# Performance work log

Hardware: AMD Instinct MI355X
Metric: run time of the kernel (lower is better)

## Reference

```python
import jax, jax.numpy as jnp
import numpy as np
from jax import lax

ALPHA = 1.5
N_ITER = 50  # entmax bisect default
GAIN = 1.414


def _p(z):
    # gp_inv(clamp(z,0), alpha) = z_+^(1/(alpha-1)) = z_+^2 for alpha=1.5
    zc = jnp.clip(z, 0.0, None)
    return zc * zc


def entmax15(X):
    """alpha-entmax (alpha=1.5) along last dim via bisection (entmax lib algorithm)."""
    d = X.shape[-1]
    Xs = X * (ALPHA - 1.0)
    mx = jnp.max(Xs, axis=-1, keepdims=True)
    tau_lo = mx - 1.0                       # gp(1, alpha) = 1
    tau_hi = mx - (1.0 / d) ** (ALPHA - 1.0)  # gp(1/d, alpha)
    f_lo = jnp.sum(_p(Xs - tau_lo), axis=-1, keepdims=True) - 1.0

    def body(i, carry):
        tau_lo, dm = carry
        dm = dm * 0.5
        tau_m = tau_lo + dm
        f_m = jnp.sum(_p(Xs - tau_m), axis=-1, keepdims=True) - 1.0
        tau_lo = jnp.where(f_m * f_lo >= 0.0, tau_m, tau_lo)
        return (tau_lo, dm)

    tau_lo, _ = lax.fori_loop(0, N_ITER, body, (tau_lo, tau_hi - tau_lo))
    p = _p(Xs - tau_lo)
    return p / jnp.sum(p, axis=-1, keepdims=True)  # ensure_sum_one=True


def _xavier(key, shape):
    std = GAIN * (2.0 / (shape[0] + shape[1])) ** 0.5
    a = (3.0 ** 0.5) * std
    return jax.random.uniform(key, shape, minval=-a, maxval=a, dtype=jnp.float32)


def setup_inputs() -> dict:
    B, F, E, N = 2048, 64, 256, 64  # batch, nfield, nemb, ncross
    key = jax.random.key(0)
    k1, k2, k3, k4 = jax.random.split(key, 4)
    return {
        "x": jax.random.normal(k1, (B, F, E), dtype=jnp.float32),
        "bilinear_w": _xavier(k2, (E, E)),
        "query": _xavier(k3, (N, E)),
        "value": _xavier(k4, (N, F)),
    }


def reference(x, bilinear_w, query, value):
    # x: [B,F,E]; bilinear_w: [E,E]; query: [N,E]; value: [N,F]
    scale = x.shape[-1] ** -0.5
    k = jnp.einsum('bfe,de->bfd', x, bilinear_w)        # [B,F,E]
    att_gate = jnp.einsum('bfd,nd->bnf', k, query) * scale  # [B,N,F]
    sparse_gate = entmax15(att_gate)                     # entmax over F
    attn_weight = sparse_gate * value[None]              # [B,N,F]
    return jnp.exp(jnp.einsum('bfe,bnf->bne', x, attn_weight))  # [B,N,E]
```

## Files before the change

kernel.cpp:

```cpp
#include <hip/hip_runtime.h>
#include <hip/hip_bf16.h>

typedef __attribute__((ext_vector_type(8))) short bf16x8;
typedef __attribute__((ext_vector_type(4))) float f32x4;

__device__ __forceinline__ unsigned short f2bf(float f) {
  unsigned int u = __float_as_uint(f);
  u += 0x7FFFu + ((u >> 16) & 1u);
  return (unsigned short)(u >> 16);
}

__global__ void __launch_bounds__(256) qw_kernel(const float* __restrict__ q,
                                                 const float* __restrict__ W,
                                                 unsigned short* __restrict__ qw) {
  int n = blockIdx.x, e = threadIdx.x;
  float acc = 0.f;
  #pragma unroll 8
  for (int d = 0; d < 256; ++d) acc = fmaf(q[n * 256 + d], W[d * 256 + e], acc);
  qw[n * 256 + e] = f2bf(acc * 0.0625f);
}

__global__ void __launch_bounds__(512, 6) cross_main(
    const float* __restrict__ x, const float* __restrict__ value,
    const unsigned short* __restrict__ qw, float* __restrict__ out) {

  __shared__ __align__(16) unsigned short lds_x[64 * 264];
  __shared__ __align__(16) unsigned char  lds_pool[64 * 68 * 4];

  float* lds_att = (float*)lds_pool;
  unsigned short* lds_aw = (unsigned short*)lds_pool;

  const int t = threadIdx.x;
  const int b = blockIdx.x;
  const int l = t & 63;
  const int w = t >> 6;
  const int l15 = l & 15, l4 = l >> 4;

  {
    const float4* xg = (const float4*)(x + (size_t)b * 16384);
    #pragma unroll
    for (int it = 0; it < 8; ++it) {
      int i = it * 512 + t;
      float4 v = xg[i];
      int f = i >> 6, c = i & 63;
      unsigned int lo = (unsigned int)f2bf(v.x) | ((unsigned int)f2bf(v.y) << 16);
      unsigned int hi = (unsigned int)f2bf(v.z) | ((unsigned int)f2bf(v.w) << 16);
      *(uint2*)&lds_x[f * 264 + 4 * c] = make_uint2(lo, hi);
    }
  }
  __syncthreads();

  {
    int nt = w >> 1, ft0 = (w & 1) * 2;
    f32x4 acc0 = {0.f, 0.f, 0.f, 0.f}, acc1 = {0.f, 0.f, 0.f, 0.f};
    const unsigned short* qa = qw + (nt * 16 + l15) * 256 + l4 * 8;
    const unsigned short* xb0 = &lds_x[(ft0 * 16 + l15) * 264 + l4 * 8];
    const unsigned short* xb1 = xb0 + 16 * 264;
    #pragma unroll
    for (int kc = 0; kc < 8; ++kc) {
      bf16x8 a  = *(const bf16x8*)(qa + kc * 32);
      bf16x8 b0 = *(const bf16x8*)(xb0 + kc * 32);
      bf16x8 b1 = *(const bf16x8*)(xb1 + kc * 32);
      acc0 = __builtin_amdgcn_mfma_f32_16x16x32_bf16(a, b0, acc0, 0, 0, 0);
      acc1 = __builtin_amdgcn_mfma_f32_16x16x32_bf16(a, b1, acc1, 0, 0, 0);
    }
    int nrow = nt * 16 + 4 * l4;
    #pragma unroll
    for (int r = 0; r < 4; ++r) {
      lds_att[(nrow + r) * 68 + ft0 * 16 + l15]       = acc0[r];
      lds_att[(nrow + r) * 68 + (ft0 + 1) * 16 + l15] = acc1[r];
    }
  }
  __syncthreads();

  {
    int n = w * 8 + (l >> 3);
    int fb = (l & 7) * 8;
    f32x4 z0 = *(const f32x4*)&lds_att[n * 68 + fb];
    f32x4 z1 = *(const f32x4*)&lds_att[n * 68 + fb + 4];
    __syncthreads();
    float z[8];
    #pragma unroll
    for (int k = 0; k < 4; ++k) { z[k] = z0[k] * 0.5f; z[k + 4] = z1[k] * 0.5f; }
    float m = z[0];
    #pragma unroll
    for (int k = 1; k < 8; ++k) m = fmaxf(m, z[k]);
    m = fmaxf(m, __shfl_xor(m, 1));
    m = fmaxf(m, __shfl_xor(m, 2));
    m = fmaxf(m, __shfl_xor(m, 4));
    float tau = m - 1.0f;
    float dm = (m - 0.125f) - tau;
    float s = 0.f;
    #pragma unroll
    for (int k = 0; k < 8; ++k) { float d = fmaxf(z[k] - tau, 0.f); s = fmaf(d, d, s); }
    s += __shfl_xor(s, 1); s += __shfl_xor(s, 2); s += __shfl_xor(s, 4);
    const float f_lo = s - 1.0f;
    for (int it = 0; it < 28; ++it) {
      dm *= 0.5f;
      float tm = tau + dm;
      float s2 = 0.f;
      #pragma unroll
      for (int k = 0; k < 8; ++k) { float d = fmaxf(z[k] - tm, 0.f); s2 = fmaf(d, d, s2); }
      s2 += __shfl_xor(s2, 1); s2 += __shfl_xor(s2, 2); s2 += __shfl_xor(s2, 4);
      if ((s2 - 1.0f) * f_lo >= 0.f) tau = tm;
    }
    float p[8]; float S = 0.f;
    #pragma unroll
    for (int k = 0; k < 8; ++k) { float d = fmaxf(z[k] - tau, 0.f); p[k] = d * d; S += p[k]; }
    S += __shfl_xor(S, 1); S += __shfl_xor(S, 2); S += __shfl_xor(S, 4);
    float invS = 1.0f / S;
    const float4* vg = (const float4*)(value + n * 64 + fb);
    float4 va = vg[0], vb = vg[1];
    union { unsigned short u[8]; bf16x8 v; } pk;
    pk.u[0] = f2bf(p[0] * invS * va.x); pk.u[1] = f2bf(p[1] * invS * va.y);
    pk.u[2] = f2bf(p[2] * invS * va.z); pk.u[3] = f2bf(p[3] * invS * va.w);
    pk.u[4] = f2bf(p[4] * invS * vb.x); pk.u[5] = f2bf(p[5] * invS * vb.y);
    pk.u[6] = f2bf(p[6] * invS * vb.z); pk.u[7] = f2bf(p[7] * invS * vb.w);
    *(bf16x8*)&lds_aw[n * 72 + fb] = pk.v;
  }
  __syncthreads();

  {
    const int te0 = 2 * w;
    f32x4 acc[4][2];
    #pragma unroll
    for (int nt = 0; nt < 4; ++nt) {
      acc[nt][0] = (f32x4){0.f, 0.f, 0.f, 0.f};
      acc[nt][1] = (f32x4){0.f, 0.f, 0.f, 0.f};
    }
    #pragma unroll
    for (int kc = 0; kc < 2; ++kc) {
      bf16x8 a[4];
      #pragma unroll
      for (int nt = 0; nt < 4; ++nt)
        a[nt] = *(const bf16x8*)&lds_aw[(nt * 16 + l15) * 72 + kc * 32 + l4 * 8];
      int f0 = kc * 32 + l4 * 8;
      #pragma unroll
      for (int j = 0; j < 2; ++j) {
        int e = (te0 + j) * 16 + l15;
        union { unsigned short u[8]; bf16x8 v; } bb;
        #pragma unroll
        for (int i = 0; i < 8; ++i) bb.u[i] = lds_x[(f0 + i) * 264 + e];
        #pragma unroll
        for (int nt = 0; nt < 4; ++nt)
          acc[nt][j] = __builtin_amdgcn_mfma_f32_16x16x32_bf16(a[nt], bb.v, acc[nt][j], 0, 0, 0);
      }
    }
    float* ob = out + (size_t)b * 16384;
    #pragma unroll
    for (int nt = 0; nt < 4; ++nt) {
      #pragma unroll
      for (int j = 0; j < 2; ++j) {
        #pragma unroll
        for (int r = 0; r < 4; ++r) {
          ob[(nt * 16 + 4 * l4 + r) * 256 + (te0 + j) * 16 + l15] = __expf(acc[nt][j][r]);
        }
      }
    }
  }
}

extern "C" void kernel_launch(void* const* d_in, const int* in_sizes, int n_in,
                              void* d_out, int out_size, void* d_ws, size_t ws_size,
                              hipStream_t stream) {
  const float* x     = (const float*)d_in[0];
  const float* W     = (const float*)d_in[1];
  const float* q     = (const float*)d_in[2];
  const float* value = (const float*)d_in[3];
  float* out = (float*)d_out;
  unsigned short* qw = (unsigned short*)d_ws;

  qw_kernel<<<dim3(64), dim3(256), 0, stream>>>(q, W, qw);
  cross_main<<<dim3(2048), dim3(512), 0, stream>>>(x, value, qw, out);
}
```

Measured before the change: 76.92 us.

## Replace entmax bisection with Newton iterations and repad x LDS tile

The 28-step bisection for the entmax threshold becomes 12 Newton-style updates. Each update uses the sum of squares and the linear sum of the clipped differences, so there are fewer iterations and fewer shuffle reductions per row. The x tile in LDS gets a row stride of 268 instead of 264, with matching 8-byte loads and stores to change bank-conflict patterns. Float-to-bf16 conversion switches to the packed intrinsic. Newton convergence from the lower bound with only 12 steps may give a threshold that differs slightly from the bisection result.

```diff
diff --git a/kernel.cpp b/kernel.cpp
--- a/kernel.cpp
+++ b/kernel.cpp
@@ -4,6 +4,11 @@
 typedef __attribute__((ext_vector_type(8))) short bf16x8;
 typedef __attribute__((ext_vector_type(4))) float f32x4;
 
+__device__ __forceinline__ unsigned int pk2(float a, float b) {
+  union { __hip_bfloat162 h; unsigned int u; } cv;
+  cv.h = __float22bfloat162_rn(make_float2(a, b));
+  return cv.u;
+}
 __device__ __forceinline__ unsigned short f2bf(float f) {
   unsigned int u = __float_as_uint(f);
   u += 0x7FFFu + ((u >> 16) & 1u);
@@ -24,7 +29,7 @@
     const float* __restrict__ x, const float* __restrict__ value,
     const unsigned short* __restrict__ qw, float* __restrict__ out) {
 
-  __shared__ __align__(16) unsigned short lds_x[64 * 264];
+  __shared__ __align__(16) unsigned short lds_x[64 * 268];
   __shared__ __align__(16) unsigned char  lds_pool[64 * 68 * 4];
 
   float* lds_att = (float*)lds_pool;
@@ -39,13 +44,13 @@
   {
     const float4* xg = (const float4*)(x + (size_t)b * 16384);
     #pragma unroll
-    for (int it = 0; it < 8; ++it) {
-      int i = it * 512 + t;
-      float4 v = xg[i];
-      int f = i >> 6, c = i & 63;
-      unsigned int lo = (unsigned int)f2bf(v.x) | ((unsigned int)f2bf(v.y) << 16);
-      unsigned int hi = (unsigned int)f2bf(v.z) | ((unsigned int)f2bf(v.w) << 16);
-      *(uint2*)&lds_x[f * 264 + 4 * c] = make_uint2(lo, hi);
+    for (int it = 0; it < 4; ++it) {
+      int u = it * 512 + t;
+      float4 v0 = xg[2 * u], v1 = xg[2 * u + 1];
+      int f = u >> 5, c8 = u & 31;
+      char* dst = (char*)lds_x + f * 536 + c8 * 16;
+      *(uint2*)dst       = make_uint2(pk2(v0.x, v0.y), pk2(v0.z, v0.w));
+      *(uint2*)(dst + 8) = make_uint2(pk2(v1.x, v1.y), pk2(v1.z, v1.w));
     }
   }
   __syncthreads();
@@ -54,15 +59,19 @@
     int nt = w >> 1, ft0 = (w & 1) * 2;
     f32x4 acc0 = {0.f, 0.f, 0.f, 0.f}, acc1 = {0.f, 0.f, 0.f, 0.f};
     const unsigned short* qa = qw + (nt * 16 + l15) * 256 + l4 * 8;
-    const unsigned short* xb0 = &lds_x[(ft0 * 16 + l15) * 264 + l4 * 8];
-    const unsigned short* xb1 = xb0 + 16 * 264;
+    const char* rb0 = (const char*)lds_x + (ft0 * 16 + l15) * 536 + l4 * 16;
+    const char* rb1 = rb0 + 16 * 536;
     #pragma unroll
     for (int kc = 0; kc < 8; ++kc) {
-      bf16x8 a  = *(const bf16x8*)(qa + kc * 32);
-      bf16x8 b0 = *(const bf16x8*)(xb0 + kc * 32);
-      bf16x8 b1 = *(const bf16x8*)(xb1 + kc * 32);
-      acc0 = __builtin_amdgcn_mfma_f32_16x16x32_bf16(a, b0, acc0, 0, 0, 0);
-      acc1 = __builtin_amdgcn_mfma_f32_16x16x32_bf16(a, b1, acc1, 0, 0, 0);
+      union BF { uint2 d[2]; bf16x8 v; };
+      bf16x8 a = *(const bf16x8*)(qa + kc * 32);
+      BF b0, b1;
+      b0.d[0] = *(const uint2*)(rb0 + kc * 64);
+      b0.d[1] = *(const uint2*)(rb0 + kc * 64 + 8);
+      b1.d[0] = *(const uint2*)(rb1 + kc * 64);
+      b1.d[1] = *(const uint2*)(rb1 + kc * 64 + 8);
+      acc0 = __builtin_amdgcn_mfma_f32_16x16x32_bf16(a, b0.v, acc0, 0, 0, 0);
+      acc1 = __builtin_amdgcn_mfma_f32_16x16x32_bf16(a, b1.v, acc1, 0, 0, 0);
     }
     int nrow = nt * 16 + 4 * l4;
     #pragma unroll
@@ -82,27 +91,26 @@
     float z[8];
     #pragma unroll
     for (int k = 0; k < 4; ++k) { z[k] = z0[k] * 0.5f; z[k + 4] = z1[k] * 0.5f; }
-    float m = z[0];
-    #pragma unroll
-    for (int k = 1; k < 8; ++k) m = fmaxf(m, z[k]);
+    float m = fmaxf(fmaxf(fmaxf(z[0], z[1]), fmaxf(z[2], z[3])),
+                    fmaxf(fmaxf(z[4], z[5]), fmaxf(z[6], z[7])));
     m = fmaxf(m, __shfl_xor(m, 1));
     m = fmaxf(m, __shfl_xor(m, 2));
     m = fmaxf(m, __shfl_xor(m, 4));
     float tau = m - 1.0f;
-    float dm = (m - 0.125f) - tau;
-    float s = 0.f;
     #pragma unroll
-    for (int k = 0; k < 8; ++k) { float d = fmaxf(z[k] - tau, 0.f); s = fmaf(d, d, s); }
-    s += __shfl_xor(s, 1); s += __shfl_xor(s, 2); s += __shfl_xor(s, 4);
-    const float f_lo = s - 1.0f;
-    for (int it = 0; it < 28; ++it) {
-      dm *= 0.5f;
-      float tm = tau + dm;
-      float s2 = 0.f;
+    for (int it = 0; it < 12; ++it) {
+      float s0 = 0.f, s1 = 0.f, q0 = 0.f, q1 = 0.f;
       #pragma unroll
-      for (int k = 0; k < 8; ++k) { float d = fmaxf(z[k] - tm, 0.f); s2 = fmaf(d, d, s2); }
-      s2 += __shfl_xor(s2, 1); s2 += __shfl_xor(s2, 2); s2 += __shfl_xor(s2, 4);
-      if ((s2 - 1.0f) * f_lo >= 0.f) tau = tm;
+      for (int k = 0; k < 4; ++k) {
+        float d0 = fmaxf(z[k] - tau, 0.f);
+        float d1 = fmaxf(z[k + 4] - tau, 0.f);
+        s0 = fmaf(d0, d0, s0); q0 += d0;
+        s1 = fmaf(d1, d1, s1); q1 += d1;
+      }
+      float s = s0 + s1, q = q0 + q1;
+      s += __shfl_xor(s, 1); s += __shfl_xor(s, 2); s += __shfl_xor(s, 4);
+      q += __shfl_xor(q, 1); q += __shfl_xor(q, 2); q += __shfl_xor(q, 4);
+      tau += (s - 1.0f) * 0.5f * __builtin_amdgcn_rcpf(q);
     }
     float p[8]; float S = 0.f;
     #pragma unroll
@@ -111,12 +119,12 @@
     float invS = 1.0f / S;
     const float4* vg = (const float4*)(value + n * 64 + fb);
     float4 va = vg[0], vb = vg[1];
-    union { unsigned short u[8]; bf16x8 v; } pk;
-    pk.u[0] = f2bf(p[0] * invS * va.x); pk.u[1] = f2bf(p[1] * invS * va.y);
-    pk.u[2] = f2bf(p[2] * invS * va.z); pk.u[3] = f2bf(p[3] * invS * va.w);
-    pk.u[4] = f2bf(p[4] * invS * vb.x); pk.u[5] = f2bf(p[5] * invS * vb.y);
-    pk.u[6] = f2bf(p[6] * invS * vb.z); pk.u[7] = f2bf(p[7] * invS * vb.w);
-    *(bf16x8*)&lds_aw[n * 72 + fb] = pk.v;
+    uint4 pkv;
+    pkv.x = pk2(p[0] * invS * va.x, p[1] * invS * va.y);
+    pkv.y = pk2(p[2] * invS * va.z, p[3] * invS * va.w);
+    pkv.z = pk2(p[4] * invS * vb.x, p[5] * invS * vb.y);
+    pkv.w = pk2(p[6] * invS * vb.z, p[7] * invS * vb.w);
+    *(uint4*)&lds_aw[n * 72 + fb] = pkv;
   }
   __syncthreads();
 
@@ -134,13 +142,13 @@
       #pragma unroll
       for (int nt = 0; nt < 4; ++nt)
         a[nt] = *(const bf16x8*)&lds_aw[(nt * 16 + l15) * 72 + kc * 32 + l4 * 8];
-      int f0 = kc * 32 + l4 * 8;
+      const char* gp = (const char*)lds_x + (kc * 32 + l4 * 8) * 536 + (te0 * 16 + l15) * 2;
       #pragma unroll
       for (int j = 0; j < 2; ++j) {
-        int e = (te0 + j) * 16 + l15;
         union { unsigned short u[8]; bf16x8 v; } bb;
         #pragma unroll
-        for (int i = 0; i < 8; ++i) bb.u[i] = lds_x[(f0 + i) * 264 + e];
+        for (int i = 0; i < 8; ++i)
+          bb.u[i] = *(const unsigned short*)(gp + i * 536 + j * 32);
         #pragma unroll
         for (int nt = 0; nt < 4; ++nt)
           acc[nt][j] = __builtin_amdgcn_mfma_f32_16x16x32_bf16(a[nt], bb.v, acc[nt][j], 0, 0, 0);
```

New measurement: 71.52 us. -7.0%, faster.
